# Kernel tuning notes

Measured on AMD Instinct MI355X. Metric: run time of the kernel, lower is better.

## Reference

```python
import jax, jax.numpy as jnp
import numpy as np

N, E, IN_DIM, HID, OUT = 50000, 800000, 128, 128, 64


def setup_inputs() -> dict:
    key = jax.random.key(0)
    k = jax.random.split(key, 6)
    h = jax.random.normal(k[0], (N, IN_DIM), dtype=jnp.float32)
    edge_index = jax.random.randint(k[1], (2, E), 0, N, dtype=jnp.int64)
    s_in, s_hid = 1.0 / np.sqrt(IN_DIM), 1.0 / np.sqrt(HID)
    W_gcn = jax.random.uniform(k[2], (IN_DIM, HID), jnp.float32, -s_in, s_in)
    b_gcn = jnp.zeros((HID,), jnp.float32)
    W_fc = jax.random.uniform(k[3], (HID, OUT), jnp.float32, -s_hid, s_hid)
    b_fc = jax.random.uniform(k[4], (OUT,), jnp.float32, -s_hid, s_hid)
    return {"h": h, "edge_index": edge_index, "W_gcn": W_gcn,
            "b_gcn": b_gcn, "W_fc": W_fc, "b_fc": b_fc}


def reference(h, edge_index, W_gcn, b_gcn, W_fc, b_fc):
    n = h.shape[0]
    # GCNConv: transform, add self-loops, symmetric normalization, scatter-add
    x = h @ W_gcn                                   # [N, HID]
    loop = jnp.arange(n, dtype=edge_index.dtype)
    row = jnp.concatenate([edge_index[0], loop])    # source nodes
    col = jnp.concatenate([edge_index[1], loop])    # destination nodes
    deg = jax.ops.segment_sum(jnp.ones_like(col, dtype=x.dtype), col,
                              num_segments=n)       # in-degree incl. self-loop
    dinv = jnp.where(deg > 0, jax.lax.rsqrt(deg), 0.0)
    norm = dinv[row] * dinv[col]                    # [E+N]
    msg = x[row] * norm[:, None]                    # gather + scale
    agg = jax.ops.segment_sum(msg, col, num_segments=n) + b_gcn
    # ReLU then projection
    return jax.nn.relu(agg) @ W_fc + b_fc
```

## Files before the change

### kernel.cpp

```cpp
#include <hip/hip_runtime.h>

#define N_NODES 50000
#define N_EDGES 800000
#define NBKT 196
#define BCAP 6144
#define UTS 136

typedef __attribute__((ext_vector_type(4))) float floatx4;
typedef __attribute__((ext_vector_type(8))) _Float16 half8;
typedef __attribute__((ext_vector_type(4))) _Float16 half4;
typedef __attribute__((ext_vector_type(2))) _Float16 half2v;

#define O_PTR   0UL
#define O_GF    200192UL
#define O_DINV  401664UL
#define O_ESRC  601856UL
#define O_W1    3801856UL
#define O_W2    3834624UL
#define O_STG   3851008UL
#define O_H16   8667904UL

__global__ __launch_bounds__(256) void k_binA(const int* __restrict__ ei,
                                              int* __restrict__ gfill,
                                              unsigned* __restrict__ staging,
                                              const float* __restrict__ Wg,
                                              const float* __restrict__ Wf,
                                              _Float16* __restrict__ W1,
                                              _Float16* __restrict__ W2) {
    int b = blockIdx.x, t = threadIdx.x;
    if (b >= NBKT) {
        int wb = b - NBKT;
        if (wb < 64) {
            int i = wb * 256 + t;
            int n = i >> 7, k = i & 127;
            W1[i] = (_Float16)Wg[k * 128 + n];
        } else {
            int i = (wb - 64) * 256 + t;
            int n = i >> 7, k = i & 127;
            W2[i] = (_Float16)Wf[k * 64 + n];
        }
        return;
    }
    __shared__ int cnt[NBKT];
    __shared__ int gbase[NBKT];
    __shared__ int s_i64;
    if (t < 64) {
        unsigned w = ((const unsigned*)ei)[2 * t + 1];
        unsigned long long m = __ballot(w == 0u);
        if (t == 0) s_i64 = (__popcll(m) >= 60) ? 1 : 0;
    }
    for (int i = t; i < NBKT; i += 256) cnt[i] = 0;
    __syncthreads();
    bool i64 = s_i64 != 0;
    int e0 = b * 4096 + t * 16;
    int sv[16], dvv[16];
    if (i64) {
        const int4* ps = (const int4*)(ei) + (e0 >> 1);
        const int4* pd = (const int4*)(ei + 2 * (size_t)N_EDGES) + (e0 >> 1);
#pragma unroll
        for (int g = 0; g < 8; ++g) {
            if (e0 + 2 * g < N_EDGES) {
                int4 s4 = ps[g], d4 = pd[g];
                sv[2 * g] = s4.x; sv[2 * g + 1] = s4.z;
                dvv[2 * g] = d4.x; dvv[2 * g + 1] = d4.z;
            } else { dvv[2 * g] = -1; dvv[2 * g + 1] = -1; }
        }
    } else {
        const int4* ps = (const int4*)(ei) + (e0 >> 2);
        const int4* pd = (const int4*)(ei + (size_t)N_EDGES) + (e0 >> 2);
#pragma unroll
        for (int g = 0; g < 4; ++g) {
            if (e0 + 4 * g < N_EDGES) {
                int4 s4 = ps[g], d4 = pd[g];
                sv[4 * g] = s4.x; sv[4 * g + 1] = s4.y; sv[4 * g + 2] = s4.z; sv[4 * g + 3] = s4.w;
                dvv[4 * g] = d4.x; dvv[4 * g + 1] = d4.y; dvv[4 * g + 2] = d4.z; dvv[4 * g + 3] = d4.w;
            } else { dvv[4 * g] = -1; dvv[4 * g + 1] = -1; dvv[4 * g + 2] = -1; dvv[4 * g + 3] = -1; }
        }
    }
    unsigned pk[16]; int rk[16]; short bk[16];
#pragma unroll
    for (int j = 0; j < 16; ++j) {
        int d = dvv[j];
        if (d >= 0 && e0 + j < N_EDGES) {
            int bkt = d >> 8;
            bk[j] = (short)bkt;
            pk[j] = (unsigned)sv[j] | ((unsigned)(d & 255) << 16);
            rk[j] = atomicAdd(&cnt[bkt], 1);
        } else bk[j] = -1;
    }
    __syncthreads();
    for (int i = t; i < NBKT; i += 256)
        gbase[i] = atomicAdd(&gfill[i], cnt[i]);
    __syncthreads();
#pragma unroll
    for (int j = 0; j < 16; ++j) {
        if (bk[j] >= 0) {
            int pos = gbase[bk[j]] + rk[j];
            if (pos < BCAP) staging[(size_t)bk[j] * BCAP + pos] = pk[j];
        }
    }
}

__global__ __launch_bounds__(256) void k_binB(const unsigned* __restrict__ staging,
                                              const int* __restrict__ gfill,
                                              int* __restrict__ ptr,
                                              float* __restrict__ dinv,
                                              int* __restrict__ esrc) {
    __shared__ unsigned se[BCAP];
    __shared__ int lcnt[256];
    __shared__ int lscan[256];
    __shared__ int cur[256];
    __shared__ int s_cb;
    int b = blockIdx.x, t = threadIdx.x;
    int nbase = b * 256;
    int nn = min(256, N_NODES - nbase);
    int cnt = min(gfill[b], BCAP);
    if (t < 64) {
        int acc = 0;
        for (int i = t; i < b; i += 64) acc += min(gfill[i], BCAP);
#pragma unroll
        for (int off = 32; off > 0; off >>= 1) acc += __shfl_down(acc, off);
        if (t == 0) s_cb = acc;
    }
    lcnt[t] = 0;
    __syncthreads();
    int cb = s_cb;
    const unsigned* st = staging + (size_t)b * BCAP;
    for (int i = t; i < cnt; i += 256) {
        unsigned p = st[i];
        se[i] = p;
        atomicAdd(&lcnt[p >> 16], 1);
    }
    __syncthreads();
    int v = lcnt[t];
    lscan[t] = v;
    __syncthreads();
    for (int off = 1; off < 256; off <<= 1) {
        int x = (t >= off) ? lscan[t - off] : 0;
        __syncthreads(); lscan[t] += x; __syncthreads();
    }
    int segstart = cb + (lscan[t] - v);
    if (t < nn) {
        int node = nbase + t;
        ptr[node] = segstart;
        dinv[node] = rsqrtf((float)(v + 1));
        cur[t] = segstart;
    }
    __syncthreads();
    for (int i = t; i < cnt; i += 256) {
        unsigned p = se[i];
        int pos = atomicAdd(&cur[p >> 16], 1);
        esrc[pos] = (int)(p & 0xffffu);
    }
}

__global__ __launch_bounds__(256) void k_conv(const float* __restrict__ h,
                                              const float* __restrict__ dinv,
                                              _Float16* __restrict__ h16) {
    __shared__ float sdv[128];
    int b = blockIdx.x, t = threadIdx.x;
    int nb = b * 128;
    int nn = min(128, N_NODES - nb);
    if (nn <= 0) return;
    if (t < nn) sdv[t] = dinv[nb + t];
    __syncthreads();
    const floatx4* src = (const floatx4*)(h + (size_t)nb * 128);
    half4* dst = (half4*)(h16 + (size_t)nb * 128);
    int nq = nn * 32;
    for (int i = t; i < nq; i += 256) {
        floatx4 v = src[i];
        float s = sdv[i >> 5];
        half4 o;
        o[0] = (_Float16)(v[0] * s); o[1] = (_Float16)(v[1] * s);
        o[2] = (_Float16)(v[2] * s); o[3] = (_Float16)(v[3] * s);
        dst[i] = o;
    }
}

__global__ __launch_bounds__(256, 8) void k_aggF(const _Float16* __restrict__ h16,
                                                 const int* __restrict__ ptr,
                                                 const int* __restrict__ esrc,
                                                 const float* __restrict__ dinv,
                                                 const _Float16* __restrict__ W1,
                                                 const _Float16* __restrict__ W2,
                                                 const float* __restrict__ bg,
                                                 const float* __restrict__ bfc,
                                                 float* __restrict__ out) {
    __shared__ _Float16 ut[16 * UTS];
    __shared__ _Float16 z[16 * UTS];
    int wave = threadIdx.x >> 6;
    int lane = threadIdx.x & 63;
    int nb = blockIdx.x * 16;
    for (int q = 0; q < 4; ++q) {
        int node = nb + wave * 4 + q;
        int p0 = ptr[node];
        int p1 = (node + 1 < N_NODES) ? ptr[node + 1] : N_EDGES;
        half2v us = *(const half2v*)(h16 + (size_t)node * 128 + lane * 2);
        float a0 = (float)us[0], a1 = (float)us[1];
        for (int base = p0; base < p1; base += 64) {
            int cnt = p1 - base; if (cnt > 64) cnt = 64;
            int idx = 0;
            if (lane < cnt) idx = esrc[base + lane];
            int j = 0;
            for (; j + 8 <= cnt; j += 8) {
                int s0 = __shfl(idx, j),     s1 = __shfl(idx, j + 1);
                int s2 = __shfl(idx, j + 2), s3 = __shfl(idx, j + 3);
                int s4 = __shfl(idx, j + 4), s5 = __shfl(idx, j + 5);
                int s6 = __shfl(idx, j + 6), s7 = __shfl(idx, j + 7);
                half2v u0 = *(const half2v*)(h16 + (size_t)s0 * 128 + lane * 2);
                half2v u1 = *(const half2v*)(h16 + (size_t)s1 * 128 + lane * 2);
                half2v u2 = *(const half2v*)(h16 + (size_t)s2 * 128 + lane * 2);
                half2v u3 = *(const half2v*)(h16 + (size_t)s3 * 128 + lane * 2);
                half2v u4 = *(const half2v*)(h16 + (size_t)s4 * 128 + lane * 2);
                half2v u5 = *(const half2v*)(h16 + (size_t)s5 * 128 + lane * 2);
                half2v u6 = *(const half2v*)(h16 + (size_t)s6 * 128 + lane * 2);
                half2v u7 = *(const half2v*)(h16 + (size_t)s7 * 128 + lane * 2);
                a0 += (float)u0[0] + (float)u1[0] + (float)u2[0] + (float)u3[0]
                    + (float)u4[0] + (float)u5[0] + (float)u6[0] + (float)u7[0];
                a1 += (float)u0[1] + (float)u1[1] + (float)u2[1] + (float)u3[1]
                    + (float)u4[1] + (float)u5[1] + (float)u6[1] + (float)u7[1];
            }
            for (; j + 4 <= cnt; j += 4) {
                int s0 = __shfl(idx, j),     s1 = __shfl(idx, j + 1);
                int s2 = __shfl(idx, j + 2), s3 = __shfl(idx, j + 3);
                half2v u0 = *(const half2v*)(h16 + (size_t)s0 * 128 + lane * 2);
                half2v u1 = *(const half2v*)(h16 + (size_t)s1 * 128 + lane * 2);
                half2v u2 = *(const half2v*)(h16 + (size_t)s2 * 128 + lane * 2);
                half2v u3 = *(const half2v*)(h16 + (size_t)s3 * 128 + lane * 2);
                a0 += (float)u0[0] + (float)u1[0] + (float)u2[0] + (float)u3[0];
                a1 += (float)u0[1] + (float)u1[1] + (float)u2[1] + (float)u3[1];
            }
            for (; j < cnt; ++j) {
                int s = __shfl(idx, j);
                half2v uu = *(const half2v*)(h16 + (size_t)s * 128 + lane * 2);
                a0 += (float)uu[0]; a1 += (float)uu[1];
            }
        }
        float sc = dinv[node];
        int r = wave * 4 + q;
        ut[r * UTS + lane * 2]     = (_Float16)(a0 * sc);
        ut[r * UTS + lane * 2 + 1] = (_Float16)(a1 * sc);
    }
    __syncthreads();
    int quad = lane >> 4, l15 = lane & 15;
    half8 a[4];
#pragma unroll
    for (int kk = 0; kk < 4; ++kk)
        a[kk] = *(const half8*)(ut + l15 * UTS + kk * 32 + quad * 8);
#pragma unroll
    for (int tt = 0; tt < 2; ++tt) {
        floatx4 acc = {0.f, 0.f, 0.f, 0.f};
        int n = (wave * 2 + tt) * 16 + l15;
#pragma unroll
        for (int kk = 0; kk < 4; ++kk) {
            half8 bb = *(const half8*)(W1 + n * 128 + kk * 32 + quad * 8);
            acc = __builtin_amdgcn_mfma_f32_16x16x32_f16(a[kk], bb, acc, 0, 0, 0);
        }
        float bias = bg[n];
#pragma unroll
        for (int i = 0; i < 4; ++i)
            z[(quad * 4 + i) * UTS + n] = (_Float16)fmaxf(acc[i] + bias, 0.f);
    }
    __syncthreads();
    half8 a2[4];
#pragma unroll
    for (int kk = 0; kk < 4; ++kk)
        a2[kk] = *(const half8*)(z + l15 * UTS + kk * 32 + quad * 8);
    {
        floatx4 acc = {0.f, 0.f, 0.f, 0.f};
        int n = wave * 16 + l15;
#pragma unroll
        for (int kk = 0; kk < 4; ++kk) {
            half8 bb = *(const half8*)(W2 + n * 128 + kk * 32 + quad * 8);
            acc = __builtin_amdgcn_mfma_f32_16x16x32_f16(a2[kk], bb, acc, 0, 0, 0);
        }
        float bias = bfc[n];
#pragma unroll
        for (int i = 0; i < 4; ++i)
            out[(size_t)(nb + quad * 4 + i) * 64 + n] = acc[i] + bias;
    }
}

extern "C" void kernel_launch(void* const* d_in, const int* in_sizes, int n_in,
                              void* d_out, int out_size, void* d_ws, size_t ws_size,
                              hipStream_t stream) {
    (void)in_sizes; (void)n_in; (void)out_size; (void)ws_size;
    const float* h  = (const float*)d_in[0];
    const int*   ei = (const int*)d_in[1];
    const float* Wg = (const float*)d_in[2];
    const float* bg = (const float*)d_in[3];
    const float* Wf = (const float*)d_in[4];
    const float* bf = (const float*)d_in[5];
    float* out = (float*)d_out;

    char* ws = (char*)d_ws;
    int*      ptr   = (int*)(ws + O_PTR);
    int*      gfill = (int*)(ws + O_GF);
    float*    dinv  = (float*)(ws + O_DINV);
    int*      esrc  = (int*)(ws + O_ESRC);
    _Float16* W1    = (_Float16*)(ws + O_W1);
    _Float16* W2    = (_Float16*)(ws + O_W2);
    unsigned* staging = (unsigned*)(ws + O_STG);
    _Float16* h16   = (_Float16*)(ws + O_H16);

    hipMemsetAsync(gfill, 0, NBKT * sizeof(int), stream);
    k_binA<<<NBKT + 96, 256, 0, stream>>>(ei, gfill, staging, Wg, Wf, W1, W2);
    k_binB<<<NBKT, 256, 0, stream>>>(staging, gfill, ptr, dinv, esrc);
    k_conv<<<(N_NODES + 127) / 128, 256, 0, stream>>>(h, dinv, h16);
    k_aggF<<<N_NODES / 16, 256, 0, stream>>>(h16, ptr, esrc, dinv,
                                             W1, W2, bg, bf, out);
}
```

Measured before the change: 161.7 us.

## Drop CSR build kernel; bin edges into 64-node buckets and sort in-block

Removes the k_binB pass that built the CSR ptr/esrc arrays and dinv. Edges are now binned into 782 buckets of 64 destination nodes. The conversion kernel recomputes degrees from the staging buckets, and the aggregation kernel sorts its 16 nodes' edges in shared memory before gathering. This saves a launch and a global round trip for esrc/ptr/dinv. In exchange, staging is scanned redundantly: 4 aggregation blocks each read a whole bucket, and the held[7] array caps a bucket at 1792 edges.

```diff
diff --git a/kernel.cpp b/kernel.cpp
--- a/kernel.cpp
+++ b/kernel.cpp
@@ -2,8 +2,9 @@
 
 #define N_NODES 50000
 #define N_EDGES 800000
-#define NBKT 196
-#define BCAP 6144
+#define NBKT 782
+#define BINB 196
+#define BCAP 1792
 #define UTS 136
 
 typedef __attribute__((ext_vector_type(4))) float floatx4;
@@ -11,25 +12,22 @@
 typedef __attribute__((ext_vector_type(4))) _Float16 half4;
 typedef __attribute__((ext_vector_type(2))) _Float16 half2v;
 
-#define O_PTR   0UL
-#define O_GF    200192UL
-#define O_DINV  401664UL
-#define O_ESRC  601856UL
-#define O_W1    3801856UL
-#define O_W2    3834624UL
-#define O_STG   3851008UL
-#define O_H16   8667904UL
-
-__global__ __launch_bounds__(256) void k_binA(const int* __restrict__ ei,
-                                              int* __restrict__ gfill,
-                                              unsigned* __restrict__ staging,
-                                              const float* __restrict__ Wg,
-                                              const float* __restrict__ Wf,
-                                              _Float16* __restrict__ W1,
-                                              _Float16* __restrict__ W2) {
+#define O_GF    0UL
+#define O_W1    3200UL
+#define O_W2    35968UL
+#define O_STG   52480UL
+#define O_H16   5657856UL
+
+__global__ __launch_bounds__(256) void k_bin(const int* __restrict__ ei,
+                                             int* __restrict__ gfill,
+                                             unsigned* __restrict__ staging,
+                                             const float* __restrict__ Wg,
+                                             const float* __restrict__ Wf,
+                                             _Float16* __restrict__ W1,
+                                             _Float16* __restrict__ W2) {
     int b = blockIdx.x, t = threadIdx.x;
-    if (b >= NBKT) {
-        int wb = b - NBKT;
+    if (b >= BINB) {
+        int wb = b - BINB;
         if (wb < 64) {
             int i = wb * 256 + t;
             int n = i >> 7, k = i & 127;
@@ -82,9 +80,9 @@
     for (int j = 0; j < 16; ++j) {
         int d = dvv[j];
         if (d >= 0 && e0 + j < N_EDGES) {
-            int bkt = d >> 8;
+            int bkt = d >> 6;
             bk[j] = (short)bkt;
-            pk[j] = (unsigned)sv[j] | ((unsigned)(d & 255) << 16);
+            pk[j] = (unsigned)sv[j] | ((unsigned)(d & 63) << 16);
             rk[j] = atomicAdd(&cnt[bkt], 1);
         } else bk[j] = -1;
     }
@@ -101,68 +99,28 @@
     }
 }
 
-__global__ __launch_bounds__(256) void k_binB(const unsigned* __restrict__ staging,
+__global__ __launch_bounds__(256) void k_conv(const float* __restrict__ h,
                                               const int* __restrict__ gfill,
-                                              int* __restrict__ ptr,
-                                              float* __restrict__ dinv,
-                                              int* __restrict__ esrc) {
-    __shared__ unsigned se[BCAP];
-    __shared__ int lcnt[256];
-    __shared__ int lscan[256];
-    __shared__ int cur[256];
-    __shared__ int s_cb;
-    int b = blockIdx.x, t = threadIdx.x;
-    int nbase = b * 256;
-    int nn = min(256, N_NODES - nbase);
-    int cnt = min(gfill[b], BCAP);
-    if (t < 64) {
-        int acc = 0;
-        for (int i = t; i < b; i += 64) acc += min(gfill[i], BCAP);
-#pragma unroll
-        for (int off = 32; off > 0; off >>= 1) acc += __shfl_down(acc, off);
-        if (t == 0) s_cb = acc;
-    }
-    lcnt[t] = 0;
-    __syncthreads();
-    int cb = s_cb;
-    const unsigned* st = staging + (size_t)b * BCAP;
-    for (int i = t; i < cnt; i += 256) {
-        unsigned p = st[i];
-        se[i] = p;
-        atomicAdd(&lcnt[p >> 16], 1);
-    }
-    __syncthreads();
-    int v = lcnt[t];
-    lscan[t] = v;
-    __syncthreads();
-    for (int off = 1; off < 256; off <<= 1) {
-        int x = (t >= off) ? lscan[t - off] : 0;
-        __syncthreads(); lscan[t] += x; __syncthreads();
-    }
-    int segstart = cb + (lscan[t] - v);
-    if (t < nn) {
-        int node = nbase + t;
-        ptr[node] = segstart;
-        dinv[node] = rsqrtf((float)(v + 1));
-        cur[t] = segstart;
-    }
-    __syncthreads();
-    for (int i = t; i < cnt; i += 256) {
-        unsigned p = se[i];
-        int pos = atomicAdd(&cur[p >> 16], 1);
-        esrc[pos] = (int)(p & 0xffffu);
-    }
-}
-
-__global__ __launch_bounds__(256) void k_conv(const float* __restrict__ h,
-                                              const float* __restrict__ dinv,
+                                              const unsigned* __restrict__ staging,
                                               _Float16* __restrict__ h16) {
+    __shared__ int deg[128];
     __shared__ float sdv[128];
     int b = blockIdx.x, t = threadIdx.x;
     int nb = b * 128;
     int nn = min(128, N_NODES - nb);
     if (nn <= 0) return;
-    if (t < nn) sdv[t] = dinv[nb + t];
+    if (t < 128) deg[t] = 0;
+    __syncthreads();
+#pragma unroll
+    for (int kb = 0; kb < 2; ++kb) {
+        int gb = b * 2 + kb;
+        int cnt = min(gfill[gb], BCAP);
+        const unsigned* st = staging + (size_t)gb * BCAP;
+        for (int i = t; i < cnt; i += 256)
+            atomicAdd(&deg[kb * 64 + (st[i] >> 16)], 1);
+    }
+    __syncthreads();
+    if (t < 128) sdv[t] = rsqrtf((float)(deg[t] + 1));
     __syncthreads();
     const floatx4* src = (const floatx4*)(h + (size_t)nb * 128);
     half4* dst = (half4*)(h16 + (size_t)nb * 128);
@@ -178,9 +136,8 @@
 }
 
 __global__ __launch_bounds__(256, 8) void k_aggF(const _Float16* __restrict__ h16,
-                                                 const int* __restrict__ ptr,
-                                                 const int* __restrict__ esrc,
-                                                 const float* __restrict__ dinv,
+                                                 const int* __restrict__ gfill,
+                                                 const unsigned* __restrict__ staging,
                                                  const _Float16* __restrict__ W1,
                                                  const _Float16* __restrict__ W2,
                                                  const float* __restrict__ bg,
@@ -188,21 +145,60 @@
                                                  float* __restrict__ out) {
     __shared__ _Float16 ut[16 * UTS];
     __shared__ _Float16 z[16 * UTS];
-    int wave = threadIdx.x >> 6;
-    int lane = threadIdx.x & 63;
+    __shared__ unsigned short se[BCAP];
+    __shared__ int deg16[16], seg16[16], cur16[16];
+    __shared__ float sdv16[16];
+    int t = threadIdx.x;
+    int wave = t >> 6;
+    int lane = t & 63;
     int nb = blockIdx.x * 16;
+    int bkt = blockIdx.x >> 2;
+    unsigned lo = (unsigned)(blockIdx.x & 3) * 16;
+    int cnt = min(gfill[bkt], BCAP);
+    if (t < 16) deg16[t] = 0;
+    __syncthreads();
+    const unsigned* st = staging + (size_t)bkt * BCAP;
+    unsigned held[7];
+#pragma unroll
+    for (int r = 0; r < 7; ++r) {
+        int i = t + r * 256;
+        unsigned p = 0xFFFFFFFFu;
+        if (i < cnt) p = st[i];
+        unsigned tg = p >> 16;
+        if (tg - lo < 16u) atomicAdd(&deg16[tg - lo], 1);
+        else p = 0xFFFFFFFFu;
+        held[r] = p;
+    }
+    __syncthreads();
+    if (t == 0) {
+        int s = 0;
+#pragma unroll
+        for (int k = 0; k < 16; ++k) { seg16[k] = s; cur16[k] = s; s += deg16[k]; }
+    }
+    if (t < 16) sdv16[t] = rsqrtf((float)(deg16[t] + 1));
+    __syncthreads();
+#pragma unroll
+    for (int r = 0; r < 7; ++r) {
+        unsigned p = held[r];
+        if (p != 0xFFFFFFFFu) {
+            int rk = atomicAdd(&cur16[(p >> 16) - lo], 1);
+            if (rk < BCAP) se[rk] = (unsigned short)(p & 0xffffu);
+        }
+    }
+    __syncthreads();
     for (int q = 0; q < 4; ++q) {
-        int node = nb + wave * 4 + q;
-        int p0 = ptr[node];
-        int p1 = (node + 1 < N_NODES) ? ptr[node + 1] : N_EDGES;
+        int tag = wave * 4 + q;
+        int node = nb + tag;
+        int p0 = seg16[tag];
+        int p1 = p0 + deg16[tag];
         half2v us = *(const half2v*)(h16 + (size_t)node * 128 + lane * 2);
         float a0 = (float)us[0], a1 = (float)us[1];
         for (int base = p0; base < p1; base += 64) {
-            int cnt = p1 - base; if (cnt > 64) cnt = 64;
+            int c = p1 - base; if (c > 64) c = 64;
             int idx = 0;
-            if (lane < cnt) idx = esrc[base + lane];
+            if (lane < c) idx = se[base + lane];
             int j = 0;
-            for (; j + 8 <= cnt; j += 8) {
+            for (; j + 8 <= c; j += 8) {
                 int s0 = __shfl(idx, j),     s1 = __shfl(idx, j + 1);
                 int s2 = __shfl(idx, j + 2), s3 = __shfl(idx, j + 3);
                 int s4 = __shfl(idx, j + 4), s5 = __shfl(idx, j + 5);
@@ -220,7 +216,7 @@
                 a1 += (float)u0[1] + (float)u1[1] + (float)u2[1] + (float)u3[1]
                     + (float)u4[1] + (float)u5[1] + (float)u6[1] + (float)u7[1];
             }
-            for (; j + 4 <= cnt; j += 4) {
+            for (; j + 4 <= c; j += 4) {
                 int s0 = __shfl(idx, j),     s1 = __shfl(idx, j + 1);
                 int s2 = __shfl(idx, j + 2), s3 = __shfl(idx, j + 3);
                 half2v u0 = *(const half2v*)(h16 + (size_t)s0 * 128 + lane * 2);
@@ -230,13 +226,13 @@
                 a0 += (float)u0[0] + (float)u1[0] + (float)u2[0] + (float)u3[0];
                 a1 += (float)u0[1] + (float)u1[1] + (float)u2[1] + (float)u3[1];
             }
-            for (; j < cnt; ++j) {
+            for (; j < c; ++j) {
                 int s = __shfl(idx, j);
                 half2v uu = *(const half2v*)(h16 + (size_t)s * 128 + lane * 2);
                 a0 += (float)uu[0]; a1 += (float)uu[1];
             }
         }
-        float sc = dinv[node];
+        float sc = sdv16[tag];
         int r = wave * 4 + q;
         ut[r * UTS + lane * 2]     = (_Float16)(a0 * sc);
         ut[r * UTS + lane * 2 + 1] = (_Float16)(a1 * sc);
@@ -294,19 +290,15 @@
     float* out = (float*)d_out;
 
     char* ws = (char*)d_ws;
-    int*      ptr   = (int*)(ws + O_PTR);
     int*      gfill = (int*)(ws + O_GF);
-    float*    dinv  = (float*)(ws + O_DINV);
-    int*      esrc  = (int*)(ws + O_ESRC);
     _Float16* W1    = (_Float16*)(ws + O_W1);
     _Float16* W2    = (_Float16*)(ws + O_W2);
     unsigned* staging = (unsigned*)(ws + O_STG);
     _Float16* h16   = (_Float16*)(ws + O_H16);
 
     hipMemsetAsync(gfill, 0, NBKT * sizeof(int), stream);
-    k_binA<<<NBKT + 96, 256, 0, stream>>>(ei, gfill, staging, Wg, Wf, W1, W2);
-    k_binB<<<NBKT, 256, 0, stream>>>(staging, gfill, ptr, dinv, esrc);
-    k_conv<<<(N_NODES + 127) / 128, 256, 0, stream>>>(h, dinv, h16);
-    k_aggF<<<N_NODES / 16, 256, 0, stream>>>(h16, ptr, esrc, dinv,
+    k_bin<<<BINB + 96, 256, 0, stream>>>(ei, gfill, staging, Wg, Wf, W1, W2);
+    k_conv<<<(N_NODES + 127) / 128, 256, 0, stream>>>(h, gfill, staging, h16);
+    k_aggF<<<N_NODES / 16, 256, 0, stream>>>(h16, gfill, staging,
                                              W1, W2, bg, bf, out);
 }
```

Result: faster. 154.1 us (-4.7%).
